# Optimization experiments

Measured on AMD Instinct MI355X. Metric: run time of the kernel, lower is better.

The kernel has to match this reference:

```python
import jax, jax.numpy as jnp
import numpy as np

H = 1024   # hidden_size
V = 50257  # output_size (vocab)
B = 64     # batch
S = 256    # encoder seq len
NE = 7     # num_emotions


def setup_inputs() -> dict:
    key = jax.random.key(0)
    ks = jax.random.split(key, 16)
    def nrm(k, shape, scale=0.02):
        return jax.random.normal(k, shape, dtype=jnp.float32) * scale
    return {
        "input_step": jax.random.randint(ks[0], (1, B), 0, V),
        "input_step_emotion": jax.random.randint(ks[1], (1, B), 0, NE),
        "last_hidden": jax.random.normal(ks[2], (1, B, H), dtype=jnp.float32),
        "input_context": jax.random.normal(ks[3], (B, H), dtype=jnp.float32),
        "encoder_outputs": jax.random.normal(ks[4], (S, B, H), dtype=jnp.float32),
        "ememory": jax.random.randint(ks[5], (V,), 0, 2).astype(jnp.int32),
        "embedding": nrm(ks[6], (V, H)),
        "emotion_embedding": nrm(ks[7], (NE, H)),
        "W_read": nrm(ks[8], (H, 3 * H)), "b_read": jnp.zeros((H,), jnp.float32),
        "W_write": nrm(ks[9], (H, H)), "b_write": jnp.zeros((H,), jnp.float32),
        "W_ih": nrm(ks[10], (3 * H, 4 * H)), "W_hh": nrm(ks[11], (3 * H, H)),
        "b_ih": jnp.zeros((3 * H,), jnp.float32), "b_hh": jnp.zeros((3 * H,), jnp.float32),
        "W_concat": nrm(ks[12], (H, 2 * H)), "b_concat": jnp.zeros((H,), jnp.float32),
        "W_out": nrm(ks[13], (V, H)), "b_out": jnp.zeros((V,), jnp.float32),
        "W_alpha": nrm(ks[14], (1, V)), "b_alpha": jnp.zeros((1,), jnp.float32),
    }


def reference(input_step, input_step_emotion, last_hidden, input_context,
              encoder_outputs, ememory, embedding, emotion_embedding,
              W_read, b_read, W_write, b_write, W_ih, W_hh, b_ih, b_hh,
              W_concat, b_concat, W_out, b_out, W_alpha, b_alpha):
    Hd = last_hidden.shape[-1]
    # ---- ECM internal memory (read gate) ----
    emo = emotion_embedding[input_step_emotion]            # [1,B,H]
    lw = embedding[input_step]                             # [1,B,H]
    h_sum = jnp.sum(last_hidden, axis=0, keepdims=True)    # [1,B,H]
    ctx_in = input_context[None]                           # [1,B,H]
    M_read = jax.nn.sigmoid(jnp.concatenate([lw, h_sum, ctx_in], -1) @ W_read.T + b_read)
    emo_g = emo * M_read                                   # gated emotion state
    # ---- single GRU step (PyTorch gate order r,z,n) ----
    X = jnp.concatenate([lw, h_sum, ctx_in, emo_g], -1)[0]  # [B,4H]
    h0 = last_hidden[0]                                     # [B,H]
    gi = X @ W_ih.T + b_ih
    gh = h0 @ W_hh.T + b_hh
    r = jax.nn.sigmoid(gi[:, :Hd] + gh[:, :Hd])
    z = jax.nn.sigmoid(gi[:, Hd:2 * Hd] + gh[:, Hd:2 * Hd])
    n = jnp.tanh(gi[:, 2 * Hd:] + r * gh[:, 2 * Hd:])
    h_new = (1.0 - z) * n + z * h0                          # [B,H]
    rnn_output = h_new[None]                                # [1,B,H]
    hidden = h_new[None]
    # ---- write gate ----
    M_write = jax.nn.sigmoid(rnn_output @ W_write.T + b_write)
    new_M_emo = emo_g * M_write                             # [1,B,H]
    # ---- Luong dot attention ----
    scores = jnp.sum(rnn_output * encoder_outputs, axis=2).T  # [B,S]
    attn_w = jax.nn.softmax(scores, axis=1)
    context = jnp.einsum('bs,sbh->bh', attn_w, encoder_outputs)  # [B,H]
    concat_out = jnp.tanh(jnp.concatenate([h_new, context], 1) @ W_concat.T + b_concat)
    # ---- external memory gated dual softmax ----
    logits = concat_out @ W_out.T + b_out                   # [B,V]
    g = jax.nn.sigmoid(logits @ W_alpha.T + b_alpha)        # [B,1]
    mask = (ememory == 1)[None]                             # [1,V]
    NEG = jnp.float32(-1e9)
    # Equivalent to torch's mask-gather -> softmax -> scatter-back-by-sorted-idx:
    # softmax within each group, reassembled in original vocab order.
    se = jax.nn.softmax(jnp.where(mask, logits, NEG), axis=1)
    sg = jax.nn.softmax(jnp.where(mask, NEG, logits), axis=1)
    output = jnp.where(mask, se * g, sg * (1.0 - g))        # [B,V]
    return (output, hidden, new_M_emo, context)
```

## Files before the change

### kernel.cpp

```cpp
#include <hip/hip_runtime.h>
#include <hip/hip_bf16.h>
#include <math.h>

#define B 64
#define H 1024
#define SEQ 256
#define V 50257
#define NBLK 786

typedef float4 f4;
typedef __attribute__((ext_vector_type(4))) float f32x4;
typedef __attribute__((ext_vector_type(8))) short bf16x8;

__device__ inline float sigm(float x){ return 1.0f/(1.0f+expf(-x)); }
__device__ inline short f2bf(float x){
  __hip_bfloat16 h = __float2bfloat16(x);
  union { __hip_bfloat16 h; short s; } u; u.h = h; return u.s;
}
__device__ inline short2 cvt2(float x, float y){
  __hip_bfloat162 h = __float22bfloat162_rn(float2{x, y});
  union { __hip_bfloat162 h; short2 s; } u; u.h = h; return u.s;
}
__device__ inline bf16x8 pack8(f4 lo, f4 hi){
  union { bf16x8 v; short2 s[4]; } u;
  u.s[0]=cvt2(lo.x,lo.y); u.s[1]=cvt2(lo.z,lo.w);
  u.s[2]=cvt2(hi.x,hi.y); u.s[3]=cvt2(hi.z,hi.w);
  return u.v;
}
__device__ inline float wrsum(float v){
  #pragma unroll
  for(int o=32;o;o>>=1) v += __shfl_xor(v,o);
  return v;
}
__device__ inline float wrmax(float v){
  #pragma unroll
  for(int o=32;o;o>>=1) v = fmaxf(v,__shfl_xor(v,o));
  return v;
}
__device__ inline f32x4 mfma16(bf16x8 a, bf16x8 b, f32x4 c){
  return __builtin_amdgcn_mfma_f32_16x16x32_bf16(a,b,c,0,0,0);
}

__global__ void k_build(const int* __restrict__ istep,
                        const float* __restrict__ lasth, const float* __restrict__ ictx,
                        const float* __restrict__ emb, short* __restrict__ X_b){
  int b = blockIdx.x; int h = threadIdx.x*4;
  int iw = istep[b];
  f4 lw = *(const f4*)(emb  + (size_t)iw*H + h);
  f4 hs = *(const f4*)(lasth + (size_t)b*H + h);
  f4 cv = *(const f4*)(ictx + (size_t)b*H + h);
  short* xb = X_b + (size_t)b*4096;
  *(short4*)(xb +        h) = make_short4(f2bf(lw.x),f2bf(lw.y),f2bf(lw.z),f2bf(lw.w));
  *(short4*)(xb + 1024 + h) = make_short4(f2bf(hs.x),f2bf(hs.y),f2bf(hs.z),f2bf(hs.w));
  *(short4*)(xb + 2048 + h) = make_short4(f2bf(cv.x),f2bf(cv.y),f2bf(cv.z),f2bf(cv.w));
}

__launch_bounds__(256)
__global__ void k_pre(const int* __restrict__ iemo, const short* __restrict__ X_b,
                      const float* __restrict__ eemb,
                      const float* __restrict__ Wread, const float* __restrict__ bread,
                      const float* __restrict__ Whh,
                      float* __restrict__ emog, short* __restrict__ X_b_w,
                      float* __restrict__ gh){
  __shared__ float red[4][64][20];
  int tid = threadIdx.x;
  int w = tid>>6, l = tid&63, lm = l&15, lq = l>>4;
  f32x4 acc0={0,0,0,0}, acc1={0,0,0,0}, acc2={0,0,0,0}, acc3={0,0,0,0};
  int readmode = (blockIdx.x < 64);
  int tile = readmode ? blockIdx.x : (blockIdx.x - 64);
  int ncol = tile*16 + lm;
  const float* wp = readmode ? (Wread + (size_t)ncol*3072 + lq*8)
                             : (Whh   + (size_t)ncol*1024 + lq*8);
  const short* ap = readmode ? (X_b + lm*4096 + lq*8)
                             : (X_b + 1024 + lm*4096 + lq*8);
  int kbeg = readmode ? w*768 : w*256;
  int kend = readmode ? (kbeg + 768) : (kbeg + 256);
  for(int k0=kbeg; k0<kend; k0+=64){
    f4 w0 = *(const f4*)(wp + k0);
    f4 w1 = *(const f4*)(wp + k0 + 4);
    f4 w2 = *(const f4*)(wp + k0 + 32);
    f4 w3 = *(const f4*)(wp + k0 + 36);
    bf16x8 a00 = *(const bf16x8*)(ap + k0);
    bf16x8 a01 = *(const bf16x8*)(ap + k0 + 32);
    bf16x8 a10 = *(const bf16x8*)(ap + 16*4096 + k0);
    bf16x8 a11 = *(const bf16x8*)(ap + 16*4096 + k0 + 32);
    bf16x8 a20 = *(const bf16x8*)(ap + 32*4096 + k0);
    bf16x8 a21 = *(const bf16x8*)(ap + 32*4096 + k0 + 32);
    bf16x8 a30 = *(const bf16x8*)(ap + 48*4096 + k0);
    bf16x8 a31 = *(const bf16x8*)(ap + 48*4096 + k0 + 32);
    bf16x8 b0 = pack8(w0,w1), b1 = pack8(w2,w3);
    acc0 = mfma16(a00,b0,acc0); acc1 = mfma16(a10,b0,acc1);
    acc2 = mfma16(a20,b0,acc2); acc3 = mfma16(a30,b0,acc3);
    acc0 = mfma16(a01,b1,acc0); acc1 = mfma16(a11,b1,acc1);
    acc2 = mfma16(a21,b1,acc2); acc3 = mfma16(a31,b1,acc3);
  }
  #pragma unroll
  for(int r=0;r<4;r++){
    red[w][     lq*4+r][lm] = acc0[r];
    red[w][16 + lq*4+r][lm] = acc1[r];
    red[w][32 + lq*4+r][lm] = acc2[r];
    red[w][48 + lq*4+r][lm] = acc3[r];
  }
  __syncthreads();
  int m = tid>>2;
  if(readmode){
    int ie = iemo[m];
    #pragma unroll
    for(int j=0;j<4;j++){
      int c = (tid&3)*4 + j;
      float v = red[0][m][c]+red[1][m][c]+red[2][m][c]+red[3][m][c];
      int n = tile*16 + c;
      float s = sigm(v + bread[n]);
      float eg = s * eemb[(size_t)ie*1024 + n];
      emog[(size_t)m*1024 + n] = eg;
      X_b_w[(size_t)m*4096 + 3072 + n] = f2bf(eg);
    }
  } else {
    #pragma unroll
    for(int j=0;j<4;j++){
      int c = (tid&3)*4 + j;
      float v = red[0][m][c]+red[1][m][c]+red[2][m][c]+red[3][m][c];
      gh[(size_t)m*3072 + tile*16 + c] = v;
    }
  }
}

__launch_bounds__(256)
__global__ void k_gi(const short* __restrict__ X_b, const float* __restrict__ Wih,
                     float* __restrict__ gp){
  __shared__ float red[4][64][20];
  int tid = threadIdx.x;
  int w = tid>>6, l = tid&63, lm = l&15, lq = l>>4;
  int half = blockIdx.y;
  int ncol = blockIdx.x*16 + lm;
  const float* wp = Wih + (size_t)ncol*4096 + lq*8;
  const short* ap = X_b + lm*4096 + lq*8;
  int kbeg = half*2048 + w*512, kend = kbeg + 512;
  f32x4 acc0={0,0,0,0}, acc1={0,0,0,0}, acc2={0,0,0,0}, acc3={0,0,0,0};
  for(int k0=kbeg; k0<kend; k0+=64){
    f4 w0 = *(const f4*)(wp + k0);
    f4 w1 = *(const f4*)(wp + k0 + 4);
    f4 w2 = *(const f4*)(wp + k0 + 32);
    f4 w3 = *(const f4*)(wp + k0 + 36);
    bf16x8 a00 = *(const bf16x8*)(ap + k0);
    bf16x8 a01 = *(const bf16x8*)(ap + k0 + 32);
    bf16x8 a10 = *(const bf16x8*)(ap + 16*4096 + k0);
    bf16x8 a11 = *(const bf16x8*)(ap + 16*4096 + k0 + 32);
    bf16x8 a20 = *(const bf16x8*)(ap + 32*4096 + k0);
    bf16x8 a21 = *(const bf16x8*)(ap + 32*4096 + k0 + 32);
    bf16x8 a30 = *(const bf16x8*)(ap + 48*4096 + k0);
    bf16x8 a31 = *(const bf16x8*)(ap + 48*4096 + k0 + 32);
    bf16x8 b0 = pack8(w0,w1), b1 = pack8(w2,w3);
    acc0 = mfma16(a00,b0,acc0); acc1 = mfma16(a10,b0,acc1);
    acc2 = mfma16(a20,b0,acc2); acc3 = mfma16(a30,b0,acc3);
    acc0 = mfma16(a01,b1,acc0); acc1 = mfma16(a11,b1,acc1);
    acc2 = mfma16(a21,b1,acc2); acc3 = mfma16(a31,b1,acc3);
  }
  #pragma unroll
  for(int r=0;r<4;r++){
    red[w][     lq*4+r][lm] = acc0[r];
    red[w][16 + lq*4+r][lm] = acc1[r];
    red[w][32 + lq*4+r][lm] = acc2[r];
    red[w][48 + lq*4+r][lm] = acc3[r];
  }
  __syncthreads();
  int m = tid>>2;
  #pragma unroll
  for(int j=0;j<4;j++){
    int c = (tid&3)*4 + j;
    float v = red[0][m][c]+red[1][m][c]+red[2][m][c]+red[3][m][c];
    gp[(size_t)(half*64+m)*3072 + blockIdx.x*16 + c] = v;
  }
}

__global__ void k_gru(const float* __restrict__ gp, const float* __restrict__ gh,
                      const float* __restrict__ bih, const float* __restrict__ bhh,
                      const float* __restrict__ h0, float* __restrict__ hid,
                      short* __restrict__ hid_b, short* __restrict__ a2_b){
  int t = blockIdx.x*256 + threadIdx.x;
  int b = t>>8, j = (t&255)*4;
  const float* gi0 = gp + (size_t)b*3072 + j;
  const float* gi1 = gp + (size_t)(64+b)*3072 + j;
  const float* ghb = gh + (size_t)b*3072 + j;
  f4 h0v = *(const f4*)(h0 + (size_t)b*1024 + j);
  f4 hres; short4 hb;
  #pragma unroll
  for(int c=0;c<4;c++){
    float r = sigm(gi0[c]      + gi1[c]      + bih[j+c]      + ghb[c]      + bhh[j+c]);
    float z = sigm(gi0[1024+c] + gi1[1024+c] + bih[1024+j+c] + ghb[1024+c] + bhh[1024+j+c]);
    float n = tanhf(gi0[2048+c] + gi1[2048+c] + bih[2048+j+c] + r*(ghb[2048+c] + bhh[2048+j+c]));
    float hv = ((const float*)&h0v)[c];
    float h = (1.0f - z)*n + z*hv;
    ((float*)&hres)[c] = h;
    ((short*)&hb)[c] = f2bf(h);
  }
  *(f4*)(hid + (size_t)b*1024 + j) = hres;
  *(short4*)(hid_b + (size_t)b*1024 + j) = hb;
  *(short4*)(a2_b + (size_t)b*2048 + j) = hb;
}

__launch_bounds__(256)
__global__ void k_flash(const float* __restrict__ enc, const float* __restrict__ hid,
                        float* __restrict__ part, float* __restrict__ ml,
                        const short* __restrict__ hid_b,
                        const float* __restrict__ Wwrite, const float* __restrict__ bwrite,
                        const float* __restrict__ emog, float* __restrict__ memo){
  __shared__ float red[4][64][20];
  int tid = threadIdx.x;
  int w = tid>>6, l = tid&63;
  if(blockIdx.x < 512){
    int b = blockIdx.x>>3, c = blockIdx.x&7;
    int chunk = c*4 + w;
    const float* hp = hid + (size_t)b*1024 + l*16;
    f4 q0 = *(const f4*)(hp), q1 = *(const f4*)(hp+4);
    f4 q2 = *(const f4*)(hp+8), q3 = *(const f4*)(hp+12);
    f4 cx0={0,0,0,0}, cx1={0,0,0,0}, cx2={0,0,0,0}, cx3={0,0,0,0};
    float mx = -1e30f, ls = 0.0f;
    int s0 = c*32 + w*8;
    for(int si=0; si<8; si++){
      const float* ep = enc + ((size_t)(s0+si)*64 + b)*1024 + l*16;
      f4 e0 = *(const f4*)(ep),   e1 = *(const f4*)(ep+4);
      f4 e2 = *(const f4*)(ep+8), e3 = *(const f4*)(ep+12);
      float d = e0.x*q0.x + e0.y*q0.y + e0.z*q0.z + e0.w*q0.w
              + e1.x*q1.x + e1.y*q1.y + e1.z*q1.z + e1.w*q1.w
              + e2.x*q2.x + e2.y*q2.y + e2.z*q2.z + e2.w*q2.w
              + e3.x*q3.x + e3.y*q3.y + e3.z*q3.z + e3.w*q3.w;
      d = wrsum(d);
      float mn = fmaxf(mx, d);
      float a = expf(mx - mn), p = expf(d - mn);
      ls = ls*a + p;
      cx0.x = cx0.x*a + p*e0.x; cx0.y = cx0.y*a + p*e0.y;
      cx0.z = cx0.z*a + p*e0.z; cx0.w = cx0.w*a + p*e0.w;
      cx1.x = cx1.x*a + p*e1.x; cx1.y = cx1.y*a + p*e1.y;
      cx1.z = cx1.z*a + p*e1.z; cx1.w = cx1.w*a + p*e1.w;
      cx2.x = cx2.x*a + p*e2.x; cx2.y = cx2.y*a + p*e2.y;
      cx2.z = cx2.z*a + p*e2.z; cx2.w = cx2.w*a + p*e2.w;
      cx3.x = cx3.x*a + p*e3.x; cx3.y = cx3.y*a + p*e3.y;
      cx3.z = cx3.z*a + p*e3.z; cx3.w = cx3.w*a + p*e3.w;
      mx = mn;
    }
    float* pp = part + ((size_t)b*32 + chunk)*1024 + l*16;
    *(f4*)(pp)    = cx0; *(f4*)(pp+4)  = cx1;
    *(f4*)(pp+8)  = cx2; *(f4*)(pp+12) = cx3;
    if(l==0){ ml[((size_t)b*32+chunk)*2] = mx; ml[((size_t)b*32+chunk)*2+1] = ls; }
  } else {
    int tile = blockIdx.x - 512;
    int lm = l&15, lq = l>>4;
    int ncol = tile*16 + lm;
    const float* wp = Wwrite + (size_t)ncol*1024 + lq*8;
    const short* ap = hid_b + lm*1024 + lq*8;
    int kbeg = w*256, kend = kbeg + 256;
    f32x4 acc0={0,0,0,0}, acc1={0,0,0,0}, acc2={0,0,0,0}, acc3={0,0,0,0};
    for(int k0=kbeg; k0<kend; k0+=64){
      f4 w0 = *(const f4*)(wp + k0);
      f4 w1 = *(const f4*)(wp + k0 + 4);
      f4 w2 = *(const f4*)(wp + k0 + 32);
      f4 w3 = *(const f4*)(wp + k0 + 36);
      bf16x8 a00 = *(const bf16x8*)(ap + k0);
      bf16x8 a01 = *(const bf16x8*)(ap + k0 + 32);
      bf16x8 a10 = *(const bf16x8*)(ap + 16*1024 + k0);
      bf16x8 a11 = *(const bf16x8*)(ap + 16*1024 + k0 + 32);
      bf16x8 a20 = *(const bf16x8*)(ap + 32*1024 + k0);
      bf16x8 a21 = *(const bf16x8*)(ap + 32*1024 + k0 + 32);
      bf16x8 a30 = *(const bf16x8*)(ap + 48*1024 + k0);
      bf16x8 a31 = *(const bf16x8*)(ap + 48*1024 + k0 + 32);
      bf16x8 b0 = pack8(w0,w1), b1 = pack8(w2,w3);
      acc0 = mfma16(a00,b0,acc0); acc1 = mfma16(a10,b0,acc1);
      acc2 = mfma16(a20,b0,acc2); acc3 = mfma16(a30,b0,acc3);
      acc0 = mfma16(a01,b1,acc0); acc1 = mfma16(a11,b1,acc1);
      acc2 = mfma16(a21,b1,acc2); acc3 = mfma16(a31,b1,acc3);
    }
    #pragma unroll
    for(int r=0;r<4;r++){
      red[w][     lq*4+r][lm] = acc0[r];
      red[w][16 + lq*4+r][lm] = acc1[r];
      red[w][32 + lq*4+r][lm] = acc2[r];
      red[w][48 + lq*4+r][lm] = acc3[r];
    }
    __syncthreads();
    int m = tid>>2;
    #pragma unroll
    for(int j=0;j<4;j++){
      int c = (tid&3)*4 + j;
      float v = red[0][m][c]+red[1][m][c]+red[2][m][c]+red[3][m][c];
      int n = tile*16 + c;
      memo[(size_t)m*1024 + n] = sigm(v + bwrite[n]) * emog[(size_t)m*1024 + n];
    }
  }
}

__global__ void k_ctxr(const float* __restrict__ part, const float* __restrict__ ml,
                       float* __restrict__ ctxo, short* __restrict__ a2_b){
  int b = blockIdx.x; int t = threadIdx.x;
  __shared__ float sscale[32];
  if(t < 64){
    float mc = (t<32) ? ml[((size_t)b*32+t)*2]   : -1e30f;
    float lc = (t<32) ? ml[((size_t)b*32+t)*2+1] : 0.0f;
    float M = wrmax(mc);
    float L = wrsum(lc * expf(mc - M));
    if(t<32) sscale[t] = expf(mc - M) / L;
  }
  __syncthreads();
  int h = t*4;
  f4 acc = {0,0,0,0};
  for(int c=0;c<32;c++){
    f4 p = *(const f4*)(part + ((size_t)b*32 + c)*1024 + h);
    float s = sscale[c];
    acc.x += s*p.x; acc.y += s*p.y; acc.z += s*p.z; acc.w += s*p.w;
  }
  *(f4*)(ctxo + (size_t)b*1024 + h) = acc;
  *(short4*)(a2_b + (size_t)b*2048 + 1024 + h) =
      make_short4(f2bf(acc.x),f2bf(acc.y),f2bf(acc.z),f2bf(acc.w));
}

__launch_bounds__(256)
__global__ void k_cc(const short* __restrict__ a2_b, const float* __restrict__ Wc,
                     const float* __restrict__ bc, short* __restrict__ cc_b){
  __shared__ float red[4][64][20];
  int tid = threadIdx.x;
  int w = tid>>6, l = tid&63, lm = l&15, lq = l>>4;
  int ncol = blockIdx.x*16 + lm;
  const float* wp = Wc + (size_t)ncol*2048 + lq*8;
  const short* ap = a2_b + lm*2048 + lq*8;
  int kbeg = w*512, kend = kbeg + 512;
  f32x4 acc0={0,0,0,0}, acc1={0,0,0,0}, acc2={0,0,0,0}, acc3={0,0,0,0};
  for(int k0=kbeg; k0<kend; k0+=64){
    f4 w0 = *(const f4*)(wp + k0);
    f4 w1 = *(const f4*)(wp + k0 + 4);
    f4 w2 = *(const f4*)(wp + k0 + 32);
    f4 w3 = *(const f4*)(wp + k0 + 36);
    bf16x8 a00 = *(const bf16x8*)(ap + k0);
    bf16x8 a01 = *(const bf16x8*)(ap + k0 + 32);
    bf16x8 a10 = *(const bf16x8*)(ap + 16*2048 + k0);
    bf16x8 a11 = *(const bf16x8*)(ap + 16*2048 + k0 + 32);
    bf16x8 a20 = *(const bf16x8*)(ap + 32*2048 + k0);
    bf16x8 a21 = *(const bf16x8*)(ap + 32*2048 + k0 + 32);
    bf16x8 a30 = *(const bf16x8*)(ap + 48*2048 + k0);
    bf16x8 a31 = *(const bf16x8*)(ap + 48*2048 + k0 + 32);
    bf16x8 b0 = pack8(w0,w1), b1 = pack8(w2,w3);
    acc0 = mfma16(a00,b0,acc0); acc1 = mfma16(a10,b0,acc1);
    acc2 = mfma16(a20,b0,acc2); acc3 = mfma16(a30,b0,acc3);
    acc0 = mfma16(a01,b1,acc0); acc1 = mfma16(a11,b1,acc1);
    acc2 = mfma16(a21,b1,acc2); acc3 = mfma16(a31,b1,acc3);
  }
  #pragma unroll
  for(int r=0;r<4;r++){
    red[w][     lq*4+r][lm] = acc0[r];
    red[w][16 + lq*4+r][lm] = acc1[r];
    red[w][32 + lq*4+r][lm] = acc2[r];
    red[w][48 + lq*4+r][lm] = acc3[r];
  }
  __syncthreads();
  int m = tid>>2;
  #pragma unroll
  for(int j=0;j<4;j++){
    int c = (tid&3)*4 + j;
    float v = red[0][m][c]+red[1][m][c]+red[2][m][c]+red[3][m][c];
    int n = blockIdx.x*16 + c;
    cc_b[(size_t)m*1024 + n] = f2bf(tanhf(v + bc[n]));
  }
}

__launch_bounds__(512)
__global__ void k_out(const short* __restrict__ A, const float* __restrict__ Wm,
                      const float* __restrict__ bias, const float* __restrict__ wal,
                      const int* __restrict__ mem,
                      float* __restrict__ outf, float* __restrict__ pstat){
  __shared__ float red[4][64][20];
  __shared__ float sst[4][64][6];
  int tid = threadIdx.x;
  int w = tid>>6, l = tid&63;
  int lm = l&15, lq = l>>4;
  int cg = w&3, half = w>>2;
  int ncol = blockIdx.x*64 + cg*16 + lm;
  int nrow = ncol < V ? ncol : V-1;
  const float* wp = Wm + (size_t)nrow*1024 + lq*8;
  const short* ap = A + lm*1024 + lq*8;
  int kbeg = half*512, kend = kbeg + 512;
  f32x4 acc0={0,0,0,0}, acc1={0,0,0,0}, acc2={0,0,0,0}, acc3={0,0,0,0};
  for(int k0=kbeg; k0<kend; k0+=64){
    f4 w0 = *(const f4*)(wp + k0);
    f4 w1 = *(const f4*)(wp + k0 + 4);
    f4 w2 = *(const f4*)(wp + k0 + 32);
    f4 w3 = *(const f4*)(wp + k0 + 36);
    bf16x8 a00 = *(const bf16x8*)(ap + k0);
    bf16x8 a01 = *(const bf16x8*)(ap + k0 + 32);
    bf16x8 a10 = *(const bf16x8*)(ap + 16*1024 + k0);
    bf16x8 a11 = *(const bf16x8*)(ap + 16*1024 + k0 + 32);
    bf16x8 a20 = *(const bf16x8*)(ap + 32*1024 + k0);
    bf16x8 a21 = *(const bf16x8*)(ap + 32*1024 + k0 + 32);
    bf16x8 a30 = *(const bf16x8*)(ap + 48*1024 + k0);
    bf16x8 a31 = *(const bf16x8*)(ap + 48*1024 + k0 + 32);
    bf16x8 b0 = pack8(w0,w1), b1 = pack8(w2,w3);
    acc0 = mfma16(a00,b0,acc0); acc1 = mfma16(a10,b0,acc1);
    acc2 = mfma16(a20,b0,acc2); acc3 = mfma16(a30,b0,acc3);
    acc0 = mfma16(a01,b1,acc0); acc1 = mfma16(a11,b1,acc1);
    acc2 = mfma16(a21,b1,acc2); acc3 = mfma16(a31,b1,acc3);
  }
  if(half==1){
    #pragma unroll
    for(int r=0;r<4;r++){
      red[cg][     lq*4+r][lm] = acc0[r];
      red[cg][16 + lq*4+r][lm] = acc1[r];
      red[cg][32 + lq*4+r][lm] = acc2[r];
      red[cg][48 + lq*4+r][lm] = acc3[r];
    }
  }
  __syncthreads();
  if(half==0){
    #pragma unroll
    for(int r=0;r<4;r++){
      acc0[r] += red[cg][     lq*4+r][lm];
      acc1[r] += red[cg][16 + lq*4+r][lm];
      acc2[r] += red[cg][32 + lq*4+r][lm];
      acc3[r] += red[cg][48 + lq*4+r][lm];
    }
    float bv=0.0f, wv=0.0f; int mv=-1;
    if(ncol < V){ bv = bias[ncol]; wv = wal[ncol]; mv = mem[ncol]; }
    #pragma unroll
    for(int qi=0; qi<4; qi++){
      #pragma unroll
      for(int r=0;r<4;r++){
        float v;
        if(qi==0) v = acc0[r]+bv; else if(qi==1) v = acc1[r]+bv;
        else if(qi==2) v = acc2[r]+bv; else v = acc3[r]+bv;
        int row = lq*4 + r + 16*qi;
        if(ncol < V) outf[(size_t)row*V + ncol] = v;
        float dd = v*wv;
        float me = (mv==1) ? v : -1e30f;
        float se = (mv==1) ? 1.0f : 0.0f;
        float mg = (mv==0) ? v : -1e30f;
        float sg = (mv==0) ? 1.0f : 0.0f;
        #pragma unroll
        for(int o=1;o<16;o<<=1){
          dd += __shfl_xor(dd,o);
          float m2=__shfl_xor(me,o), s2=__shfl_xor(se,o);
          float nm=fmaxf(me,m2); se = se*expf(me-nm) + s2*expf(m2-nm); me = nm;
          m2=__shfl_xor(mg,o); s2=__shfl_xor(sg,o);
          nm=fmaxf(mg,m2); sg = sg*expf(mg-nm) + s2*expf(m2-nm); mg = nm;
        }
        if(lm==0){
          sst[cg][row][0]=dd; sst[cg][row][1]=me; sst[cg][row][2]=se;
          sst[cg][row][3]=mg; sst[cg][row][4]=sg;
        }
      }
    }
  }
  __syncthreads();
  if(tid < 64){
    float dd=0.0f, me=-1e30f, se=0.0f, mg=-1e30f, sg=0.0f;
    #pragma unroll
    for(int g=0; g<4; g++){
      dd += sst[g][tid][0];
      float m2=sst[g][tid][1], s2=sst[g][tid][2];
      float nm=fmaxf(me,m2); se = se*expf(me-nm) + s2*expf(m2-nm); me = nm;
      m2=sst[g][tid][3]; s2=sst[g][tid][4];
      nm=fmaxf(mg,m2); sg = sg*expf(mg-nm) + s2*expf(m2-nm); mg = nm;
    }
    float* pp = pstat + ((size_t)tid*NBLK + blockIdx.x)*6;
    pp[0]=dd; pp[1]=me; pp[2]=se; pp[3]=mg; pp[4]=sg;
  }
}

__global__ void k_merge(const float* __restrict__ pstat, float* __restrict__ stats){
  int b = blockIdx.x, t = threadIdx.x;
  float dd=0.0f, me=-1e30f, se=0.0f, mg=-1e30f, sg=0.0f;
  for(int i=t; i<NBLK; i+=256){
    const float* pp = pstat + ((size_t)b*NBLK + i)*6;
    dd += pp[0];
    float m2=pp[1], s2=pp[2];
    float nm=fmaxf(me,m2); se = se*expf(me-nm) + s2*expf(m2-nm); me = nm;
    m2=pp[3]; s2=pp[4];
    nm=fmaxf(mg,m2); sg = sg*expf(mg-nm) + s2*expf(m2-nm); mg = nm;
  }
  #pragma unroll
  for(int o=32;o;o>>=1){
    dd += __shfl_xor(dd,o);
    float m2=__shfl_xor(me,o), s2=__shfl_xor(se,o);
    float nm=fmaxf(me,m2); se = se*expf(me-nm) + s2*expf(m2-nm); me = nm;
    m2=__shfl_xor(mg,o); s2=__shfl_xor(sg,o);
    nm=fmaxf(mg,m2); sg = sg*expf(mg-nm) + s2*expf(m2-nm); mg = nm;
  }
  __shared__ float sm[4][5];
  int wv = t>>6;
  if((t&63)==0){ sm[wv][0]=dd; sm[wv][1]=me; sm[wv][2]=se; sm[wv][3]=mg; sm[wv][4]=sg; }
  __syncthreads();
  if(t==0){
    float D=0, M=-1e30f, S=0, M2=-1e30f, S2=0;
    for(int i=0;i<4;i++){
      D += sm[i][0];
      float m = fmaxf(M, sm[i][1]); S  = S*expf(M-m)  + sm[i][2]*expf(sm[i][1]-m);  M = m;
      float n = fmaxf(M2,sm[i][3]); S2 = S2*expf(M2-n)+ sm[i][4]*expf(sm[i][3]-n); M2 = n;
    }
    stats[b*8+0]=D; stats[b*8+1]=M; stats[b*8+2]=M2; stats[b*8+3]=S; stats[b*8+4]=S2;
  }
}

__global__ void k_final(float* __restrict__ logits, const int* __restrict__ mem,
                        const float* __restrict__ stats, const float* __restrict__ balpha){
  int v = blockIdx.x*256 + threadIdx.x;
  int b = blockIdx.y;
  if(v >= V) return;
  float dot = stats[b*8+0], me = stats[b*8+1], mg = stats[b*8+2];
  float se = stats[b*8+3],  sg = stats[b*8+4];
  float g = sigm(dot + balpha[0]);
  float l = logits[(size_t)b*V + v];
  float o = (mem[v]==1) ? (expf(l-me)/se * g) : (expf(l-mg)/sg * (1.0f-g));
  logits[(size_t)b*V + v] = o;
}

extern "C" void kernel_launch(void* const* d_in, const int* in_sizes, int n_in,
                              void* d_out, int out_size, void* d_ws, size_t ws_size,
                              hipStream_t stream){
  const int*   istep   = (const int*)d_in[0];
  const int*   iemo    = (const int*)d_in[1];
  const float* lasth   = (const float*)d_in[2];
  const float* ictx    = (const float*)d_in[3];
  const float* enc     = (const float*)d_in[4];
  const int*   emem    = (const int*)d_in[5];
  const float* emb     = (const float*)d_in[6];
  const float* eemb    = (const float*)d_in[7];
  const float* W_read  = (const float*)d_in[8];
  const float* b_read  = (const float*)d_in[9];
  const float* W_write = (const float*)d_in[10];
  const float* b_write = (const float*)d_in[11];
  const float* W_ih    = (const float*)d_in[12];
  const float* W_hh    = (const float*)d_in[13];
  const float* b_ih    = (const float*)d_in[14];
  const float* b_hh    = (const float*)d_in[15];
  const float* W_concat= (const float*)d_in[16];
  const float* b_concat= (const float*)d_in[17];
  const float* W_out   = (const float*)d_in[18];
  const float* b_out   = (const float*)d_in[19];
  const float* W_alpha = (const float*)d_in[20];
  const float* b_alpha = (const float*)d_in[21];

  short* X_b  = (short*)d_ws;
  float* emog = (float*)((char*)d_ws + 524288);
  float* gp   = emog + 65536;
  float* gh   = gp + 393216;
  float* part = gh + 196608;
  float* ml   = part + 2097152;
  float* stats= ml + 4096;
  float* pstat= stats + 512;
  short* hid_b= (short*)(pstat + 64*NBLK*6);
  short* a2_b = hid_b + 65536;
  short* cc_b = a2_b + 131072;

  float* out0 = (float*)d_out;
  float* hid  = out0 + (size_t)B*V;
  float* memo = hid + 65536;
  float* ctxo = memo + 65536;

  k_build<<<64,256,0,stream>>>(istep, lasth, ictx, emb, X_b);
  k_pre  <<<256,256,0,stream>>>(iemo, X_b, eemb, W_read, b_read, W_hh, emog, X_b, gh);
  k_gi   <<<dim3(192,2),256,0,stream>>>(X_b, W_ih, gp);
  k_gru  <<<64,256,0,stream>>>(gp, gh, b_ih, b_hh, lasth, hid, hid_b, a2_b);
  k_flash<<<576,256,0,stream>>>(enc, hid, part, ml, hid_b, W_write, b_write, emog, memo);
  k_ctxr <<<64,256,0,stream>>>(part, ml, ctxo, a2_b);
  k_cc   <<<64,256,0,stream>>>(a2_b, W_concat, b_concat, cc_b);
  k_out  <<<NBLK,512,0,stream>>>(cc_b, W_out, b_out, W_alpha, emem, out0, pstat);
  k_merge<<<64,256,0,stream>>>(pstat, stats);
  k_final<<<dim3(197,64),256,0,stream>>>(out0, emem, stats, b_alpha);
}
```

Before: 226.9 us.

## Stage W_out tiles through double-buffered LDS with coalesced loads in k_out

k_out now loads W_out rows cooperatively into a double-buffered shared-memory tile of 64 rows by 128 columns, using coalesced float4 reads, and prefetches the next K chunk while the MFMAs run on the current one. The block shrinks from 512 to 256 threads and each wave covers the full K range, which removes the split-K LDS reduction. The aim is better global-load coalescing for the dominant 200MB fp32 weight stream and overlap of loads with compute. In exchange it uses about 67KB of LDS per block, which reduces occupancy, and it adds a barrier per K step.

```diff
diff --git a/kernel.cpp b/kernel.cpp
--- a/kernel.cpp
+++ b/kernel.cpp
@@ -361,88 +361,100 @@
   }
 }
 
-__launch_bounds__(512)
+__launch_bounds__(256)
 __global__ void k_out(const short* __restrict__ A, const float* __restrict__ Wm,
                       const float* __restrict__ bias, const float* __restrict__ wal,
                       const int* __restrict__ mem,
                       float* __restrict__ outf, float* __restrict__ pstat){
-  __shared__ float red[4][64][20];
+  __shared__ float wt[2][64][132];
   __shared__ float sst[4][64][6];
   int tid = threadIdx.x;
   int w = tid>>6, l = tid&63;
   int lm = l&15, lq = l>>4;
-  int cg = w&3, half = w>>2;
-  int ncol = blockIdx.x*64 + cg*16 + lm;
-  int nrow = ncol < V ? ncol : V-1;
-  const float* wp = Wm + (size_t)nrow*1024 + lq*8;
+  int n0 = blockIdx.x*64;
+  int ncol = n0 + w*16 + lm;
+  int fr = w*16 + lm;
   const short* ap = A + lm*1024 + lq*8;
-  int kbeg = half*512, kend = kbeg + 512;
   f32x4 acc0={0,0,0,0}, acc1={0,0,0,0}, acc2={0,0,0,0}, acc3={0,0,0,0};
-  for(int k0=kbeg; k0<kend; k0+=64){
-    f4 w0 = *(const f4*)(wp + k0);
-    f4 w1 = *(const f4*)(wp + k0 + 4);
-    f4 w2 = *(const f4*)(wp + k0 + 32);
-    f4 w3 = *(const f4*)(wp + k0 + 36);
-    bf16x8 a00 = *(const bf16x8*)(ap + k0);
-    bf16x8 a01 = *(const bf16x8*)(ap + k0 + 32);
-    bf16x8 a10 = *(const bf16x8*)(ap + 16*1024 + k0);
-    bf16x8 a11 = *(const bf16x8*)(ap + 16*1024 + k0 + 32);
-    bf16x8 a20 = *(const bf16x8*)(ap + 32*1024 + k0);
-    bf16x8 a21 = *(const bf16x8*)(ap + 32*1024 + k0 + 32);
-    bf16x8 a30 = *(const bf16x8*)(ap + 48*1024 + k0);
-    bf16x8 a31 = *(const bf16x8*)(ap + 48*1024 + k0 + 32);
-    bf16x8 b0 = pack8(w0,w1), b1 = pack8(w2,w3);
-    acc0 = mfma16(a00,b0,acc0); acc1 = mfma16(a10,b0,acc1);
-    acc2 = mfma16(a20,b0,acc2); acc3 = mfma16(a30,b0,acc3);
-    acc0 = mfma16(a01,b1,acc0); acc1 = mfma16(a11,b1,acc1);
-    acc2 = mfma16(a21,b1,acc2); acc3 = mfma16(a31,b1,acc3);
-  }
-  if(half==1){
+
+  {
+    #pragma unroll
+    for(int c=0;c<8;c++){
+      int idx = c*256 + tid;
+      int row = idx>>5, kc = idx&31;
+      int srow = n0 + row; if(srow > V-1) srow = V-1;
+      f4 v = *(const f4*)(Wm + (size_t)srow*1024 + kc*4);
+      *(f4*)(&wt[0][row][kc*4]) = v;
+    }
+  }
+  __syncthreads();
+
+  int buf = 0;
+  for(int step=0; step<8; step++){
+    if(step < 7){
+      int k0n = (step+1)*128;
+      #pragma unroll
+      for(int c=0;c<8;c++){
+        int idx = c*256 + tid;
+        int row = idx>>5, kc = idx&31;
+        int srow = n0 + row; if(srow > V-1) srow = V-1;
+        f4 v = *(const f4*)(Wm + (size_t)srow*1024 + k0n + kc*4);
+        *(f4*)(&wt[buf^1][row][kc*4]) = v;
+      }
+    }
+    int kg = step*128;
+    #pragma unroll
+    for(int kk=0; kk<128; kk+=64){
+      f4 lo0 = *(const f4*)(&wt[buf][fr][kk + lq*8]);
+      f4 hi0 = *(const f4*)(&wt[buf][fr][kk + lq*8 + 4]);
+      f4 lo1 = *(const f4*)(&wt[buf][fr][kk + 32 + lq*8]);
+      f4 hi1 = *(const f4*)(&wt[buf][fr][kk + 36 + lq*8]);
+      bf16x8 b0 = pack8(lo0,hi0), b1 = pack8(lo1,hi1);
+      int ka = kg + kk;
+      bf16x8 a00 = *(const bf16x8*)(ap + ka);
+      bf16x8 a01 = *(const bf16x8*)(ap + ka + 32);
+      bf16x8 a10 = *(const bf16x8*)(ap + 16*1024 + ka);
+      bf16x8 a11 = *(const bf16x8*)(ap + 16*1024 + ka + 32);
+      bf16x8 a20 = *(const bf16x8*)(ap + 32*1024 + ka);
+      bf16x8 a21 = *(const bf16x8*)(ap + 32*1024 + ka + 32);
+      bf16x8 a30 = *(const bf16x8*)(ap + 48*1024 + ka);
+      bf16x8 a31 = *(const bf16x8*)(ap + 48*1024 + ka + 32);
+      acc0 = mfma16(a00,b0,acc0); acc1 = mfma16(a10,b0,acc1);
+      acc2 = mfma16(a20,b0,acc2); acc3 = mfma16(a30,b0,acc3);
+      acc0 = mfma16(a01,b1,acc0); acc1 = mfma16(a11,b1,acc1);
+      acc2 = mfma16(a21,b1,acc2); acc3 = mfma16(a31,b1,acc3);
+    }
+    __syncthreads();
+    buf ^= 1;
+  }
+
+  float bv=0.0f, wv=0.0f; int mv=-1;
+  if(ncol < V){ bv = bias[ncol]; wv = wal[ncol]; mv = mem[ncol]; }
+  #pragma unroll
+  for(int qi=0; qi<4; qi++){
     #pragma unroll
     for(int r=0;r<4;r++){
-      red[cg][     lq*4+r][lm] = acc0[r];
-      red[cg][16 + lq*4+r][lm] = acc1[r];
-      red[cg][32 + lq*4+r][lm] = acc2[r];
-      red[cg][48 + lq*4+r][lm] = acc3[r];
-    }
-  }
-  __syncthreads();
-  if(half==0){
-    #pragma unroll
-    for(int r=0;r<4;r++){
-      acc0[r] += red[cg][     lq*4+r][lm];
-      acc1[r] += red[cg][16 + lq*4+r][lm];
-      acc2[r] += red[cg][32 + lq*4+r][lm];
-      acc3[r] += red[cg][48 + lq*4+r][lm];
-    }
-    float bv=0.0f, wv=0.0f; int mv=-1;
-    if(ncol < V){ bv = bias[ncol]; wv = wal[ncol]; mv = mem[ncol]; }
-    #pragma unroll
-    for(int qi=0; qi<4; qi++){
+      float v;
+      if(qi==0) v = acc0[r]+bv; else if(qi==1) v = acc1[r]+bv;
+      else if(qi==2) v = acc2[r]+bv; else v = acc3[r]+bv;
+      int row = lq*4 + r + 16*qi;
+      if(ncol < V) outf[(size_t)row*V + ncol] = v;
+      float dd = v*wv;
+      float me = (mv==1) ? v : -1e30f;
+      float se = (mv==1) ? 1.0f : 0.0f;
+      float mg = (mv==0) ? v : -1e30f;
+      float sg = (mv==0) ? 1.0f : 0.0f;
       #pragma unroll
-      for(int r=0;r<4;r++){
-        float v;
-        if(qi==0) v = acc0[r]+bv; else if(qi==1) v = acc1[r]+bv;
-        else if(qi==2) v = acc2[r]+bv; else v = acc3[r]+bv;
-        int row = lq*4 + r + 16*qi;
-        if(ncol < V) outf[(size_t)row*V + ncol] = v;
-        float dd = v*wv;
-        float me = (mv==1) ? v : -1e30f;
-        float se = (mv==1) ? 1.0f : 0.0f;
-        float mg = (mv==0) ? v : -1e30f;
-        float sg = (mv==0) ? 1.0f : 0.0f;
-        #pragma unroll
-        for(int o=1;o<16;o<<=1){
-          dd += __shfl_xor(dd,o);
-          float m2=__shfl_xor(me,o), s2=__shfl_xor(se,o);
-          float nm=fmaxf(me,m2); se = se*expf(me-nm) + s2*expf(m2-nm); me = nm;
-          m2=__shfl_xor(mg,o); s2=__shfl_xor(sg,o);
-          nm=fmaxf(mg,m2); sg = sg*expf(mg-nm) + s2*expf(m2-nm); mg = nm;
-        }
-        if(lm==0){
-          sst[cg][row][0]=dd; sst[cg][row][1]=me; sst[cg][row][2]=se;
-          sst[cg][row][3]=mg; sst[cg][row][4]=sg;
-        }
+      for(int o=1;o<16;o<<=1){
+        dd += __shfl_xor(dd,o);
+        float m2=__shfl_xor(me,o), s2=__shfl_xor(se,o);
+        float nm=fmaxf(me,m2); se = se*expf(me-nm) + s2*expf(m2-nm); me = nm;
+        m2=__shfl_xor(mg,o); s2=__shfl_xor(sg,o);
+        nm=fmaxf(mg,m2); sg = sg*expf(mg-nm) + s2*expf(m2-nm); mg = nm;
+      }
+      if(lm==0){
+        sst[w][row][0]=dd; sst[w][row][1]=me; sst[w][row][2]=se;
+        sst[w][row][3]=mg; sst[w][row][4]=sg;
       }
     }
   }
@@ -559,7 +571,7 @@
   k_flash<<<576,256,0,stream>>>(enc, hid, part, ml, hid_b, W_write, b_write, emog, memo);
   k_ctxr <<<64,256,0,stream>>>(part, ml, ctxo, a2_b);
   k_cc   <<<64,256,0,stream>>>(a2_b, W_concat, b_concat, cc_b);
-  k_out  <<<NBLK,512,0,stream>>>(cc_b, W_out, b_out, W_alpha, emem, out0, pstat);
+  k_out  <<<NBLK,256,0,stream>>>(cc_b, W_out, b_out, W_alpha, emem, out0, pstat);
   k_merge<<<64,256,0,stream>>>(pstat, stats);
   k_final<<<dim3(197,64),256,0,stream>>>(out0, emem, stats, b_alpha);
 }
```

Result: faster. 218.8 us (-3.6%).

## Restructure output GEMM: per-wave batch rows with register-resident A, no split-K

Applied to the files above, without the earlier changes.

The vocab projection kernel drops its split-K layout across 8 waves, where each wave owned 16 columns and all 64 batch rows. Now each of 4 waves owns 16 batch rows, keeps that A slice in registers across the full K, and walks the block's 4 column groups in turn. This removes the LDS split-K reduction, the cross-wave stat reduction and both block barriers. The per-row max/sum-exp stats use a two-pass max-then-sum shuffle instead of pairwise online merges. In exchange each wave re-reads the fp32 W_out rows, since every wave loads all 64 columns. It also holds 32 bf16x8 registers for A, which raises register pressure and lowers occupancy.

```diff
diff --git a/kernel.cpp b/kernel.cpp
--- a/kernel.cpp
+++ b/kernel.cpp
@@ -361,104 +361,75 @@
   }
 }
 
-__launch_bounds__(512)
+__launch_bounds__(256)
 __global__ void k_out(const short* __restrict__ A, const float* __restrict__ Wm,
                       const float* __restrict__ bias, const float* __restrict__ wal,
                       const int* __restrict__ mem,
                       float* __restrict__ outf, float* __restrict__ pstat){
-  __shared__ float red[4][64][20];
-  __shared__ float sst[4][64][6];
   int tid = threadIdx.x;
   int w = tid>>6, l = tid&63;
   int lm = l&15, lq = l>>4;
-  int cg = w&3, half = w>>2;
-  int ncol = blockIdx.x*64 + cg*16 + lm;
-  int nrow = ncol < V ? ncol : V-1;
-  const float* wp = Wm + (size_t)nrow*1024 + lq*8;
-  const short* ap = A + lm*1024 + lq*8;
-  int kbeg = half*512, kend = kbeg + 512;
-  f32x4 acc0={0,0,0,0}, acc1={0,0,0,0}, acc2={0,0,0,0}, acc3={0,0,0,0};
-  for(int k0=kbeg; k0<kend; k0+=64){
-    f4 w0 = *(const f4*)(wp + k0);
-    f4 w1 = *(const f4*)(wp + k0 + 4);
-    f4 w2 = *(const f4*)(wp + k0 + 32);
-    f4 w3 = *(const f4*)(wp + k0 + 36);
-    bf16x8 a00 = *(const bf16x8*)(ap + k0);
-    bf16x8 a01 = *(const bf16x8*)(ap + k0 + 32);
-    bf16x8 a10 = *(const bf16x8*)(ap + 16*1024 + k0);
-    bf16x8 a11 = *(const bf16x8*)(ap + 16*1024 + k0 + 32);
-    bf16x8 a20 = *(const bf16x8*)(ap + 32*1024 + k0);
-    bf16x8 a21 = *(const bf16x8*)(ap + 32*1024 + k0 + 32);
-    bf16x8 a30 = *(const bf16x8*)(ap + 48*1024 + k0);
-    bf16x8 a31 = *(const bf16x8*)(ap + 48*1024 + k0 + 32);
-    bf16x8 b0 = pack8(w0,w1), b1 = pack8(w2,w3);
-    acc0 = mfma16(a00,b0,acc0); acc1 = mfma16(a10,b0,acc1);
-    acc2 = mfma16(a20,b0,acc2); acc3 = mfma16(a30,b0,acc3);
-    acc0 = mfma16(a01,b1,acc0); acc1 = mfma16(a11,b1,acc1);
-    acc2 = mfma16(a21,b1,acc2); acc3 = mfma16(a31,b1,acc3);
-  }
-  if(half==1){
-    #pragma unroll
-    for(int r=0;r<4;r++){
-      red[cg][     lq*4+r][lm] = acc0[r];
-      red[cg][16 + lq*4+r][lm] = acc1[r];
-      red[cg][32 + lq*4+r][lm] = acc2[r];
-      red[cg][48 + lq*4+r][lm] = acc3[r];
-    }
-  }
-  __syncthreads();
-  if(half==0){
-    #pragma unroll
-    for(int r=0;r<4;r++){
-      acc0[r] += red[cg][     lq*4+r][lm];
-      acc1[r] += red[cg][16 + lq*4+r][lm];
-      acc2[r] += red[cg][32 + lq*4+r][lm];
-      acc3[r] += red[cg][48 + lq*4+r][lm];
+  int n0 = blockIdx.x*64;
+
+  bf16x8 aR[32];
+  {
+    const short* ap = A + (w*16 + lm)*1024 + lq*8;
+    #pragma unroll
+    for(int ks=0; ks<32; ks++) aR[ks] = *(const bf16x8*)(ap + ks*32);
+  }
+
+  float rdd[4]={0,0,0,0};
+  float rme[4]={-1e30f,-1e30f,-1e30f,-1e30f}, rse[4]={0,0,0,0};
+  float rmg[4]={-1e30f,-1e30f,-1e30f,-1e30f}, rsg[4]={0,0,0,0};
+
+  for(int cg=0; cg<4; cg++){
+    int ncol = n0 + cg*16 + lm;
+    int nrow = ncol < V ? ncol : V-1;
+    const float* wp = Wm + (size_t)nrow*1024 + lq*8;
+    f32x4 acc = {0,0,0,0};
+    #pragma unroll
+    for(int ks=0; ks<32; ks++){
+      f4 lo = *(const f4*)(wp + ks*32);
+      f4 hi = *(const f4*)(wp + ks*32 + 4);
+      acc = mfma16(aR[ks], pack8(lo,hi), acc);
     }
     float bv=0.0f, wv=0.0f; int mv=-1;
     if(ncol < V){ bv = bias[ncol]; wv = wal[ncol]; mv = mem[ncol]; }
     #pragma unroll
-    for(int qi=0; qi<4; qi++){
+    for(int r=0;r<4;r++){
+      float v = acc[r] + bv;
+      int row = w*16 + lq*4 + r;
+      if(ncol < V) outf[(size_t)row*V + ncol] = v;
+      float dd = v*wv;
+      float em = (mv==1) ? v : -1e30f;
+      float gm = (mv==0) ? v : -1e30f;
       #pragma unroll
-      for(int r=0;r<4;r++){
-        float v;
-        if(qi==0) v = acc0[r]+bv; else if(qi==1) v = acc1[r]+bv;
-        else if(qi==2) v = acc2[r]+bv; else v = acc3[r]+bv;
-        int row = lq*4 + r + 16*qi;
-        if(ncol < V) outf[(size_t)row*V + ncol] = v;
-        float dd = v*wv;
-        float me = (mv==1) ? v : -1e30f;
-        float se = (mv==1) ? 1.0f : 0.0f;
-        float mg = (mv==0) ? v : -1e30f;
-        float sg = (mv==0) ? 1.0f : 0.0f;
-        #pragma unroll
-        for(int o=1;o<16;o<<=1){
-          dd += __shfl_xor(dd,o);
-          float m2=__shfl_xor(me,o), s2=__shfl_xor(se,o);
-          float nm=fmaxf(me,m2); se = se*expf(me-nm) + s2*expf(m2-nm); me = nm;
-          m2=__shfl_xor(mg,o); s2=__shfl_xor(sg,o);
-          nm=fmaxf(mg,m2); sg = sg*expf(mg-nm) + s2*expf(m2-nm); mg = nm;
-        }
-        if(lm==0){
-          sst[cg][row][0]=dd; sst[cg][row][1]=me; sst[cg][row][2]=se;
-          sst[cg][row][3]=mg; sst[cg][row][4]=sg;
-        }
+      for(int o=1;o<16;o<<=1){
+        dd += __shfl_xor(dd,o);
+        em = fmaxf(em, __shfl_xor(em,o));
+        gm = fmaxf(gm, __shfl_xor(gm,o));
       }
-    }
-  }
-  __syncthreads();
-  if(tid < 64){
-    float dd=0.0f, me=-1e30f, se=0.0f, mg=-1e30f, sg=0.0f;
-    #pragma unroll
-    for(int g=0; g<4; g++){
-      dd += sst[g][tid][0];
-      float m2=sst[g][tid][1], s2=sst[g][tid][2];
-      float nm=fmaxf(me,m2); se = se*expf(me-nm) + s2*expf(m2-nm); me = nm;
-      m2=sst[g][tid][3]; s2=sst[g][tid][4];
-      nm=fmaxf(mg,m2); sg = sg*expf(mg-nm) + s2*expf(m2-nm); mg = nm;
-    }
-    float* pp = pstat + ((size_t)tid*NBLK + blockIdx.x)*6;
-    pp[0]=dd; pp[1]=me; pp[2]=se; pp[3]=mg; pp[4]=sg;
+      float pe = (mv==1) ? expf(v - em) : 0.0f;
+      float pg = (mv==0) ? expf(v - gm) : 0.0f;
+      #pragma unroll
+      for(int o=1;o<16;o<<=1){
+        pe += __shfl_xor(pe,o);
+        pg += __shfl_xor(pg,o);
+      }
+      rdd[r] += dd;
+      float nm = fmaxf(rme[r], em);
+      rse[r] = rse[r]*expf(rme[r]-nm) + pe*expf(em-nm); rme[r] = nm;
+      nm = fmaxf(rmg[r], gm);
+      rsg[r] = rsg[r]*expf(rmg[r]-nm) + pg*expf(gm-nm); rmg[r] = nm;
+    }
+  }
+  if(lm==0){
+    #pragma unroll
+    for(int r=0;r<4;r++){
+      int row = w*16 + lq*4 + r;
+      float* pp = pstat + ((size_t)row*NBLK + blockIdx.x)*6;
+      pp[0]=rdd[r]; pp[1]=rme[r]; pp[2]=rse[r]; pp[3]=rmg[r]; pp[4]=rsg[r];
+    }
   }
 }
 
@@ -559,7 +530,7 @@
   k_flash<<<576,256,0,stream>>>(enc, hid, part, ml, hid_b, W_write, b_write, emog, memo);
   k_ctxr <<<64,256,0,stream>>>(part, ml, ctxo, a2_b);
   k_cc   <<<64,256,0,stream>>>(a2_b, W_concat, b_concat, cc_b);
-  k_out  <<<NBLK,512,0,stream>>>(cc_b, W_out, b_out, W_alpha, emem, out0, pstat);
+  k_out  <<<NBLK,256,0,stream>>>(cc_b, W_out, b_out, W_alpha, emem, out0, pstat);
   k_merge<<<64,256,0,stream>>>(pstat, stats);
   k_final<<<dim3(197,64),256,0,stream>>>(out0, emem, stats, b_alpha);
 }
```

Measured after the change: 302.8 us. 1.33x slower.

## Pre-convert W_out to bf16 in the attention kernel; simplify masked softmax stats

Applied to the files above, without the earlier changes.

Extra blocks appended to the attention/write-gate kernel convert the full fp32 W_out matrix to bf16 in workspace. The vocab projection then reads bf16 weights directly instead of loading fp32 and packing per tile. The per-column softmax statistics switch from an online max/sum merge over shuffles to two passes: a max reduction, then a reduction of exponentials. The conversion runs on every call, adding a full fp32 read and a bf16 write of the largest matrix, so total memory traffic rises unless the conversion overlaps well with the attention work.

```diff
diff --git a/kernel.cpp b/kernel.cpp
--- a/kernel.cpp
+++ b/kernel.cpp
@@ -204,7 +204,8 @@
                         float* __restrict__ part, float* __restrict__ ml,
                         const short* __restrict__ hid_b,
                         const float* __restrict__ Wwrite, const float* __restrict__ bwrite,
-                        const float* __restrict__ emog, float* __restrict__ memo){
+                        const float* __restrict__ emog, float* __restrict__ memo,
+                        const float* __restrict__ Wout, short* __restrict__ wb){
   __shared__ float red[4][64][20];
   int tid = threadIdx.x;
   int w = tid>>6, l = tid&63;
@@ -243,7 +244,7 @@
     *(f4*)(pp)    = cx0; *(f4*)(pp+4)  = cx1;
     *(f4*)(pp+8)  = cx2; *(f4*)(pp+12) = cx3;
     if(l==0){ ml[((size_t)b*32+chunk)*2] = mx; ml[((size_t)b*32+chunk)*2+1] = ls; }
-  } else {
+  } else if(blockIdx.x < 576){
     int tile = blockIdx.x - 512;
     int lm = l&15, lq = l>>4;
     int ncol = tile*16 + lm;
@@ -285,6 +286,21 @@
       float v = red[0][m][c]+red[1][m][c]+red[2][m][c]+red[3][m][c];
       int n = tile*16 + c;
       memo[(size_t)m*1024 + n] = sigm(v + bwrite[n]) * emog[(size_t)m*1024 + n];
+    }
+  } else {
+    int tile = blockIdx.x - 576;
+    const float* src = Wout + (size_t)tile*65536;
+    short* dst = wb + (size_t)tile*65536;
+    int rbase = tile*64;
+    #pragma unroll 4
+    for(int i=0;i<64;i++){
+      int j = i*256 + tid;
+      int row = rbase + (j>>8);
+      if(row < V){
+        f4 v = *(const f4*)(src + (size_t)j*4);
+        *(short4*)(dst + (size_t)j*4) =
+            make_short4(f2bf(v.x),f2bf(v.y),f2bf(v.z),f2bf(v.w));
+      }
     }
   }
 }
@@ -362,7 +378,7 @@
 }
 
 __launch_bounds__(512)
-__global__ void k_out(const short* __restrict__ A, const float* __restrict__ Wm,
+__global__ void k_out(const short* __restrict__ A, const short* __restrict__ Wb,
                       const float* __restrict__ bias, const float* __restrict__ wal,
                       const int* __restrict__ mem,
                       float* __restrict__ outf, float* __restrict__ pstat){
@@ -374,15 +390,13 @@
   int cg = w&3, half = w>>2;
   int ncol = blockIdx.x*64 + cg*16 + lm;
   int nrow = ncol < V ? ncol : V-1;
-  const float* wp = Wm + (size_t)nrow*1024 + lq*8;
+  const short* wp = Wb + (size_t)nrow*1024 + lq*8;
   const short* ap = A + lm*1024 + lq*8;
   int kbeg = half*512, kend = kbeg + 512;
   f32x4 acc0={0,0,0,0}, acc1={0,0,0,0}, acc2={0,0,0,0}, acc3={0,0,0,0};
   for(int k0=kbeg; k0<kend; k0+=64){
-    f4 w0 = *(const f4*)(wp + k0);
-    f4 w1 = *(const f4*)(wp + k0 + 4);
-    f4 w2 = *(const f4*)(wp + k0 + 32);
-    f4 w3 = *(const f4*)(wp + k0 + 36);
+    bf16x8 b0 = *(const bf16x8*)(wp + k0);
+    bf16x8 b1 = *(const bf16x8*)(wp + k0 + 32);
     bf16x8 a00 = *(const bf16x8*)(ap + k0);
     bf16x8 a01 = *(const bf16x8*)(ap + k0 + 32);
     bf16x8 a10 = *(const bf16x8*)(ap + 16*1024 + k0);
@@ -391,7 +405,6 @@
     bf16x8 a21 = *(const bf16x8*)(ap + 32*1024 + k0 + 32);
     bf16x8 a30 = *(const bf16x8*)(ap + 48*1024 + k0);
     bf16x8 a31 = *(const bf16x8*)(ap + 48*1024 + k0 + 32);
-    bf16x8 b0 = pack8(w0,w1), b1 = pack8(w2,w3);
     acc0 = mfma16(a00,b0,acc0); acc1 = mfma16(a10,b0,acc1);
     acc2 = mfma16(a20,b0,acc2); acc3 = mfma16(a30,b0,acc3);
     acc0 = mfma16(a01,b1,acc0); acc1 = mfma16(a11,b1,acc1);
@@ -427,21 +440,24 @@
         int row = lq*4 + r + 16*qi;
         if(ncol < V) outf[(size_t)row*V + ncol] = v;
         float dd = v*wv;
-        float me = (mv==1) ? v : -1e30f;
-        float se = (mv==1) ? 1.0f : 0.0f;
-        float mg = (mv==0) ? v : -1e30f;
-        float sg = (mv==0) ? 1.0f : 0.0f;
+        float em = (mv==1) ? v : -1e30f;
+        float gm = (mv==0) ? v : -1e30f;
         #pragma unroll
         for(int o=1;o<16;o<<=1){
           dd += __shfl_xor(dd,o);
-          float m2=__shfl_xor(me,o), s2=__shfl_xor(se,o);
-          float nm=fmaxf(me,m2); se = se*expf(me-nm) + s2*expf(m2-nm); me = nm;
-          m2=__shfl_xor(mg,o); s2=__shfl_xor(sg,o);
-          nm=fmaxf(mg,m2); sg = sg*expf(mg-nm) + s2*expf(m2-nm); mg = nm;
+          em = fmaxf(em, __shfl_xor(em,o));
+          gm = fmaxf(gm, __shfl_xor(gm,o));
+        }
+        float pe = (mv==1) ? expf(v - em) : 0.0f;
+        float pg = (mv==0) ? expf(v - gm) : 0.0f;
+        #pragma unroll
+        for(int o=1;o<16;o<<=1){
+          pe += __shfl_xor(pe,o);
+          pg += __shfl_xor(pg,o);
         }
         if(lm==0){
-          sst[cg][row][0]=dd; sst[cg][row][1]=me; sst[cg][row][2]=se;
-          sst[cg][row][3]=mg; sst[cg][row][4]=sg;
+          sst[cg][row][0]=dd; sst[cg][row][1]=em; sst[cg][row][2]=pe;
+          sst[cg][row][3]=gm; sst[cg][row][4]=pg;
         }
       }
     }
@@ -546,6 +562,7 @@
   short* hid_b= (short*)(pstat + 64*NBLK*6);
   short* a2_b = hid_b + 65536;
   short* cc_b = a2_b + 131072;
+  short* wb   = cc_b + 65536;
 
   float* out0 = (float*)d_out;
   float* hid  = out0 + (size_t)B*V;
@@ -556,10 +573,11 @@
   k_pre  <<<256,256,0,stream>>>(iemo, X_b, eemb, W_read, b_read, W_hh, emog, X_b, gh);
   k_gi   <<<dim3(192,2),256,0,stream>>>(X_b, W_ih, gp);
   k_gru  <<<64,256,0,stream>>>(gp, gh, b_ih, b_hh, lasth, hid, hid_b, a2_b);
-  k_flash<<<576,256,0,stream>>>(enc, hid, part, ml, hid_b, W_write, b_write, emog, memo);
+  k_flash<<<576+NBLK,256,0,stream>>>(enc, hid, part, ml, hid_b, W_write, b_write,
+                                     emog, memo, W_out, wb);
   k_ctxr <<<64,256,0,stream>>>(part, ml, ctxo, a2_b);
   k_cc   <<<64,256,0,stream>>>(a2_b, W_concat, b_concat, cc_b);
-  k_out  <<<NBLK,512,0,stream>>>(cc_b, W_out, b_out, W_alpha, emem, out0, pstat);
+  k_out  <<<NBLK,512,0,stream>>>(cc_b, wb, b_out, W_alpha, emem, out0, pstat);
   k_merge<<<64,256,0,stream>>>(pstat, stats);
   k_final<<<dim3(197,64),256,0,stream>>>(out0, emem, stats, b_alpha);
 }
```

Result: slower. 261.7 us (+15.3%).
